# Performance work log

Measured on AMD Instinct MI355X. Metric: run time of the kernel, lower is better.

The kernel has to match this reference:

```python
import jax, jax.numpy as jnp
import numpy as np

B, S, N, H = 1024, 256, 64, 256
DA, DR = 350, 30  # attention dims W_s1 out, W_s2 out


def setup_inputs() -> dict:
    key = jax.random.key(0)
    ks = jax.random.split(key, 30)
    f32 = jnp.float32
    inp = {}
    inp['values'] = jax.random.normal(ks[0], (B, S, N), dtype=f32)
    inp['masks'] = (jax.random.uniform(ks[1], (B, S, N)) < 0.8).astype(f32)
    inp['deltas'] = jax.random.uniform(ks[2], (B, S, N), dtype=f32) * 5.0
    inp['labels'] = (jax.random.uniform(ks[3], (B,)) < 0.5).astype(f32)
    inp['is_train'] = (jax.random.uniform(ks[4], (B,)) < 0.9).astype(f32)

    def lin(k, o, i, s=0.05):
        kw, kb = jax.random.split(k)
        return (jax.random.normal(kw, (o, i), dtype=f32) * s,
                jax.random.normal(kb, (o,), dtype=f32) * s)

    inp['td_h_W'], inp['td_h_b'] = lin(ks[5], H, N)
    inp['td_x_W'], inp['td_x_b'] = lin(ks[6], N, N)
    inp['hist_W'], inp['hist_b'] = lin(ks[7], N, H)
    inp['feat_W'], inp['feat_b'] = lin(ks[8], N, N)
    inp['comb_W'], inp['comb_b'] = lin(ks[9], N, 2 * N)
    inp['W_ih'], inp['b_ih'] = lin(ks[10], 4 * H, 2 * N)
    inp['W_hh'], inp['b_hh'] = lin(ks[11], 4 * H, H)
    inp['Ws1_W'], inp['Ws1_b'] = lin(ks[12], DA, H)
    inp['Ws2_W'], inp['Ws2_b'] = lin(ks[13], DR, DA)
    inp['out_W'], inp['out_b'] = lin(ks[14], 1, DR * H)
    return inp


def reference(values, masks, deltas, labels, is_train,
              td_h_W, td_h_b, td_x_W, td_x_b,
              hist_W, hist_b, feat_W, feat_b,
              comb_W, comb_b, W_ih, W_hh, b_ih, b_hh,
              Ws1_W, Ws1_b, Ws2_W, Ws2_b, out_W, out_b):
    eye = jnp.eye(N, dtype=values.dtype)
    td_x_Wd = td_x_W * eye          # diag=True temporal decay
    feat_Wm = feat_W * (1.0 - eye)

    def step(carry, xs):
        h, c, xl = carry
        x, m, d = xs  # each [B, N]
        gamma_h = jnp.exp(-jax.nn.relu(d @ td_h_W.T + td_h_b))
        gamma_x = jnp.exp(-jax.nn.relu(d @ td_x_Wd.T + td_x_b))
        h = h * gamma_h
        x_h = h @ hist_W.T + hist_b
        msum = jnp.sum(m) + 1e-5
        xl = xl + jnp.sum(jnp.abs(x - x_h) * m) / msum
        x_c = m * x + (1.0 - m) * x_h
        z_h = x_c @ feat_Wm.T + feat_b
        xl = xl + jnp.sum(jnp.abs(x - z_h) * m) / msum
        alpha = jnp.concatenate([gamma_x, m], axis=1) @ comb_W.T + comb_b
        c_h = alpha * z_h + (1.0 - alpha) * x_h
        xl = xl + jnp.sum(jnp.abs(x - c_h) * m) / msum
        c_c = m * x + (1.0 - m) * c_h
        inp = jnp.concatenate([c_c, m], axis=1)
        gates = inp @ W_ih.T + b_ih + h @ W_hh.T + b_hh
        i_g, f_g, g_g, o_g = jnp.split(gates, 4, axis=1)  # torch LSTM gate order
        c = jax.nn.sigmoid(f_g) * c + jax.nn.sigmoid(i_g) * jnp.tanh(g_g)
        h = jax.nn.sigmoid(o_g) * jnp.tanh(c)
        return (h, c, xl), (h, c_c)

    h0 = jnp.zeros((B, H), dtype=values.dtype)
    c0 = jnp.zeros((B, H), dtype=values.dtype)
    xs = (values.transpose(1, 0, 2), masks.transpose(1, 0, 2), deltas.transpose(1, 0, 2))
    (_, _, x_loss), (Hs, imps) = jax.lax.scan(step, (h0, c0, jnp.zeros((), values.dtype)), xs)
    H_rnn = Hs.transpose(1, 0, 2)        # [B, S, H]
    imputations = imps.transpose(1, 0, 2)  # [B, S, N]

    # late attention
    scores = jnp.tanh(H_rnn @ Ws1_W.T + Ws1_b) @ Ws2_W.T + Ws2_b  # [B, S, DR]
    attn = jax.nn.softmax(scores.transpose(0, 2, 1), axis=2)       # [B, DR, S]
    hidden = jnp.einsum('brs,bsh->brh', attn, H_rnn)               # [B, DR, H]
    y_h = hidden.reshape(B, DR * H) @ out_W.T + out_b               # [B, 1]

    lab = labels.reshape(-1, 1)
    tr = is_train.reshape(-1, 1)
    bce = jax.nn.relu(y_h) - y_h * lab + jnp.log1p(jnp.exp(-jnp.abs(y_h)))
    y_loss = jnp.sum(bce * tr) / (jnp.sum(tr) + 1e-5)
    loss = x_loss / S + y_loss * 0.1
    predictions = jax.nn.sigmoid(y_h)
    return loss, predictions, imputations
```

## Files before the change

kernel.cpp:

```cpp
#include <hip/hip_runtime.h>
#include <hip/hip_bf16.h>
#include <math.h>


#define BB 1024
#define SS 256
#define NF 64
#define HD 256
#define DAA 350
#define DRR 30
#define RPB 4

#define WS_B5_OFS 4096
#define WS_B5_ELEMS (64 * 12 * 64 * 8)
#define WS_B6_OFS (WS_B5_OFS + WS_B5_ELEMS * 2)
#define WS_B6_ELEMS (22 * 8 * 64 * 8)
#define WS_B3_OFS (WS_B6_OFS + WS_B6_ELEMS * 2)
#define WS_B3_ELEMS (4 * 8 * 64 * 8)
#define WS_B2_OFS (WS_B3_OFS + WS_B3_ELEMS * 2)
#define WS_B2_ELEMS (16 * 2 * 64 * 8)
#define WS_B7_OFS (WS_B2_OFS + WS_B2_ELEMS * 2)
#define WS_B7_ELEMS (2 * 11 * 64 * 8)
#define CW_TOTAL (WS_B5_ELEMS + WS_B6_ELEMS + WS_B3_ELEMS + WS_B2_ELEMS + WS_B7_ELEMS)
#define WS_H_OFS (2 * 1024 * 1024)
#define WS_H_BYTES ((size_t)BB * SS * HD * 2)

typedef __attribute__((ext_vector_type(8))) short bf16x8;
typedef __attribute__((ext_vector_type(4))) float f32x4;

__device__ __forceinline__ float dot4f(float4 a, float4 b) {
  return fmaf(a.x, b.x, fmaf(a.y, b.y, fmaf(a.z, b.z, a.w * b.w)));
}

__device__ __forceinline__ short f2bs(float v) {
  __hip_bfloat16 t = __float2bfloat16(v);
  return *reinterpret_cast<short*>(&t);
}

__global__ __launch_bounds__(256) void convert_weights(
    const float* __restrict__ W_ih, const float* __restrict__ W_hh,
    const float* __restrict__ Ws1_W, const float* __restrict__ hist_W,
    const float* __restrict__ td_h_W, const float* __restrict__ Ws2_W,
    short* __restrict__ b5, short* __restrict__ b6,
    short* __restrict__ b3, short* __restrict__ b2, short* __restrict__ b7)
{
  int idx = blockIdx.x * 256 + threadIdx.x;
  if (idx < WS_B5_ELEMS) {
    int j = idx & 7; int e8 = idx >> 3; int lane = e8 & 63; int tile = e8 >> 6;
    int kt = tile % 12, nt = tile / 12;
    int g = nt * 16 + (lane & 15);
    int k = kt * 32 + (lane >> 4) * 8 + j;
    float v = (k < 128) ? W_ih[g * 128 + k] : W_hh[g * 256 + (k - 128)];
    b5[idx] = f2bs(v);
  } else if (idx < WS_B5_ELEMS + WS_B6_ELEMS) {
    int i = idx - WS_B5_ELEMS;
    int j = i & 7; int e8 = i >> 3; int lane = e8 & 63; int tile = e8 >> 6;
    int kt = tile & 7, nt = tile >> 3;
    int a = nt * 16 + (lane & 15);
    int k = kt * 32 + (lane >> 4) * 8 + j;
    float v = (a < DAA) ? Ws1_W[a * 256 + k] : 0.f;
    b6[i] = f2bs(v);
  } else if (idx < WS_B5_ELEMS + WS_B6_ELEMS + WS_B3_ELEMS) {
    int i = idx - WS_B5_ELEMS - WS_B6_ELEMS;
    int j = i & 7; int e8 = i >> 3; int lane = e8 & 63; int tile = e8 >> 6;
    int kt = tile & 7, nt = tile >> 3;
    int n = nt * 16 + (lane & 15);
    int k = kt * 32 + (lane >> 4) * 8 + j;
    b3[i] = f2bs(hist_W[n * 256 + k]);
  } else if (idx < WS_B5_ELEMS + WS_B6_ELEMS + WS_B3_ELEMS + WS_B2_ELEMS) {
    int i = idx - WS_B5_ELEMS - WS_B6_ELEMS - WS_B3_ELEMS;
    int j = i & 7; int e8 = i >> 3; int lane = e8 & 63; int tile = e8 >> 6;
    int kt = tile & 1, nt = tile >> 1;
    int g = nt * 16 + (lane & 15);
    int k = kt * 32 + (lane >> 4) * 8 + j;
    b2[i] = f2bs(td_h_W[g * 64 + k]);
  } else if (idx < CW_TOTAL) {
    int i = idx - WS_B5_ELEMS - WS_B6_ELEMS - WS_B3_ELEMS - WS_B2_ELEMS;
    int j = i & 7; int e8 = i >> 3; int lane = e8 & 63; int tile = e8 >> 6;
    int kt = tile % 11, nt = tile / 11;
    int r = nt * 16 + (lane & 15);
    int k = kt * 32 + (lane >> 4) * 8 + j;
    float v = (r < DRR && k < DAA) ? Ws2_W[r * DAA + k] : 0.f;
    b7[i] = f2bs(v);
  }
}

__global__ __launch_bounds__(256) void prep_kernel(
    const float* __restrict__ masks, const float* __restrict__ is_train,
    float* __restrict__ ws)
{
  __shared__ float red[256];
  const int t = blockIdx.x;
  const int tid = threadIdx.x;
  float s = 0.f;
  for (int idx = tid; idx < BB * NF; idx += 256) {
    int b = idx >> 6, n = idx & 63;
    s += masks[(size_t)b * (SS * NF) + (size_t)t * NF + n];
  }
  red[tid] = s;
  __syncthreads();
  for (int off = 128; off > 0; off >>= 1) {
    if (tid < off) red[tid] += red[tid + off];
    __syncthreads();
  }
  if (tid == 0) ws[16 + t] = red[0] + 1e-5f;
  if (blockIdx.x == 0) {
    __syncthreads();
    float ts = 0.f;
    for (int idx = tid; idx < BB; idx += 256) ts += is_train[idx];
    red[tid] = ts;
    __syncthreads();
    for (int off = 128; off > 0; off >>= 1) {
      if (tid < off) red[tid] += red[tid + off];
      __syncthreads();
    }
    if (tid == 0) { ws[2] = red[0]; ws[0] = 0.f; ws[1] = 0.f; }
  }
}

__global__ __launch_bounds__(512, 2) void rits_scan(
    const float* __restrict__ values, const float* __restrict__ masks_g,
    const float* __restrict__ deltas,
    const float* __restrict__ td_h_b, const float* __restrict__ td_x_W,
    const float* __restrict__ td_x_b, const float* __restrict__ hist_b,
    const float* __restrict__ feat_W, const float* __restrict__ feat_b,
    const float* __restrict__ comb_W, const float* __restrict__ comb_b,
    const float* __restrict__ b_ih, const float* __restrict__ b_hh,
    float* __restrict__ out, float* __restrict__ ws)
{
  __shared__ __align__(16) float sh_a[RPB][384];
  __shared__ __align__(16) short sh_ab[16][392];
  __shared__ __align__(16) short sh_db[16][72];
  __shared__ __align__(16) float sh_x[RPB][NF];
  __shared__ __align__(16) float sh_d[RPB][NF];
  __shared__ __align__(16) float sh_xc[RPB][NF];
  __shared__ __align__(16) float sh_gx[RPB][NF];
  __shared__ __align__(16) float sh_xh[RPB][NF];
  __shared__ __align__(16) float sh_gates[RPB][1024];
  __shared__ float sh_msum;

  const int tid = threadIdx.x;
  const int b0 = blockIdx.x * RPB;
  const int wv = tid >> 6;
  const int lane = tid & 63;
  const int lm = lane & 15;
  const int lq = lane >> 4;
  const int row = tid >> 7;
  const int j = tid & 127;
  const int jA = j, jB = j + 128;
  const int row2 = tid >> 6;
  const int nn = tid & 63;

  const bf16x8* b5 = (const bf16x8*)((const char*)ws + WS_B5_OFS);
  const bf16x8* b3 = (const bf16x8*)((const char*)ws + WS_B3_OFS);
  const bf16x8* b2 = (const bf16x8*)((const char*)ws + WS_B2_OFS);
  short* Hw = (short*)((char*)ws + WS_H_OFS);

  for (int i = tid; i < 16 * 392; i += 512) (&sh_ab[0][0])[i] = 0;
  for (int i = tid; i < 16 * 72; i += 512) (&sh_db[0][0])[i] = 0;
  for (int i = tid; i < RPB * 384; i += 512) (&sh_a[0][0])[i] = 0.f;

  const float tdxw  = td_x_W[nn * NF + nn];
  const float tdxb  = td_x_b[nn];
  const float featb = feat_b[nn];
  const float featd = feat_W[nn * NF + nn];
  const float combb = comb_b[nn];
  float bgA[4], bgB[4];
  #pragma unroll
  for (int q = 0; q < 4; ++q) {
    bgA[q] = b_ih[q * 256 + jA] + b_hh[q * 256 + jA];
    bgB[q] = b_ih[q * 256 + jB] + b_hh[q * 256 + jB];
  }
  float thb[2];
  thb[0] = td_h_b[(wv * 2 + 0) * 16 + lm];
  thb[1] = td_h_b[(wv * 2 + 1) * 16 + lm];
  float hbv = 0.f;
  if (wv < 4) hbv = hist_b[wv * 16 + lm];

  float cA = 0.f, cB = 0.f;
  double lossAcc = 0.0;

  float pv_a = 0.f, pv_b = 0.f, pv_msum = 0.f;
  if (tid < 256) {
    size_t g = (size_t)(b0 + row2) * (SS * NF) + nn;
    pv_a = values[g];
    pv_b = deltas[g];
  } else {
    int q = tid - 256; int rw = q >> 6, n2 = q & 63;
    size_t g = (size_t)(b0 + rw) * (SS * NF) + n2;
    pv_a = masks_g[g];
  }
  if (tid == 0) pv_msum = ws[16];

  __syncthreads();

  for (int t = 0; t < SS; ++t) {
    if (tid < 256) {
      sh_x[row2][nn] = pv_a;
      sh_d[row2][nn] = pv_b;
      sh_db[row2][nn] = f2bs(pv_b);
    } else {
      int q = tid - 256;
      int rw = q >> 6, n2 = q & 63;
      sh_a[rw][64 + n2] = pv_a;
      sh_ab[rw][64 + n2] = f2bs(pv_a);
    }
    if (tid == 0) sh_msum = pv_msum;
    __syncthreads();

    if (t + 1 < SS) {
      if (tid < 256) {
        size_t g = (size_t)(b0 + row2) * (SS * NF) + (size_t)(t + 1) * NF + nn;
        pv_a = values[g];
        pv_b = deltas[g];
      } else {
        int q = tid - 256; int rw = q >> 6, n2 = q & 63;
        size_t g = (size_t)(b0 + rw) * (SS * NF) + (size_t)(t + 1) * NF + n2;
        pv_a = masks_g[g];
      }
      if (tid == 0) pv_msum = ws[16 + t + 1];
    }

    {
      bf16x8 dfr[2];
      #pragma unroll
      for (int kt = 0; kt < 2; ++kt)
        dfr[kt] = *(const bf16x8*)(&sh_db[lm][0] + kt * 32 + lq * 8);
      #pragma unroll
      for (int ntl = 0; ntl < 2; ++ntl) {
        int nt = wv * 2 + ntl;
        f32x4 acc = {0.f, 0.f, 0.f, 0.f};
        const bf16x8* bp = b2 + (size_t)(nt * 2) * 64 + lane;
        acc = __builtin_amdgcn_mfma_f32_16x16x32_bf16(dfr[0], bp[0], acc, 0, 0, 0);
        acc = __builtin_amdgcn_mfma_f32_16x16x32_bf16(dfr[1], bp[64], acc, 0, 0, 0);
        if (lq == 0) {
          int g = nt * 16 + lm;
          float bias = thb[ntl];
          #pragma unroll
          for (int r = 0; r < 4; ++r) {
            float gam = expf(-fmaxf(acc[r] + bias, 0.f));
            float h = sh_a[r][128 + g] * gam;
            sh_a[r][128 + g] = h;
            sh_ab[r][128 + g] = f2bs(h);
          }
        }
      }
      if (tid < 256) {
        float v = sh_d[row2][nn] * tdxw + tdxb;
        sh_gx[row2][nn] = expf(-fmaxf(v, 0.f));
      }
    }
    __syncthreads();

    if (wv < 4) {
      int nt = wv;
      f32x4 acc = {0.f, 0.f, 0.f, 0.f};
      const bf16x8* bp = b3 + (size_t)(nt * 8) * 64 + lane;
      #pragma unroll
      for (int kt = 0; kt < 8; ++kt) {
        bf16x8 a = *(const bf16x8*)(&sh_ab[lm][128] + kt * 32 + lq * 8);
        acc = __builtin_amdgcn_mfma_f32_16x16x32_bf16(a, bp[kt * 64], acc, 0, 0, 0);
      }
      if (lq == 0) {
        int n = nt * 16 + lm;
        float lterm = 0.f;
        #pragma unroll
        for (int r = 0; r < 4; ++r) {
          float xh = acc[r] + hbv;
          sh_xh[r][n] = xh;
          float m = sh_a[r][64 + n], x = sh_x[r][n];
          sh_xc[r][n] = m * x + (1.f - m) * xh;
          lterm += fabsf(x - xh) * m;
        }
        lossAcc += (double)(lterm / sh_msum);
      }
    }
    __syncthreads();

    if (tid < 256) {
      const float4* xc4 = (const float4*)&sh_xc[row2][0];
      const float4* gx4 = (const float4*)&sh_gx[row2][0];
      const float4* mm4 = (const float4*)&sh_a[row2][64];
      const float4* fW  = (const float4*)(feat_W + nn * NF);
      const float4* cW0 = (const float4*)(comb_W + nn * 2 * NF);
      const float4* cW1 = (const float4*)(comb_W + nn * 2 * NF + NF);
      float az = 0.f, aa = 0.f;
      #pragma unroll
      for (int k = 0; k < 16; ++k) {
        az += dot4f(xc4[k], fW[k]);
        aa += dot4f(gx4[k], cW0[k]);
        aa += dot4f(mm4[k], cW1[k]);
      }
      float xcn = sh_xc[row2][nn];
      float zh = az - xcn * featd + featb;
      float alpha = aa + combb;
      float xh = sh_xh[row2][nn];
      float chv = alpha * zh + (1.f - alpha) * xh;
      float m = sh_a[row2][64 + nn], x = sh_x[row2][nn];
      float ccv = m * x + (1.f - m) * chv;
      sh_ab[row2][nn] = f2bs(ccv);
      out[1 + BB + ((size_t)(b0 + row2) * SS + t) * NF + nn] = ccv;
      float lsum = (fabsf(x - zh) + fabsf(x - chv)) * m;
      lossAcc += (double)(lsum / sh_msum);
    }
    __syncthreads();

    {
      bf16x8 afr[12];
      #pragma unroll
      for (int kt = 0; kt < 12; ++kt)
        afr[kt] = *(const bf16x8*)(&sh_ab[lm][0] + kt * 32 + lq * 8);
      #pragma unroll 2
      for (int ntl = 0; ntl < 8; ++ntl) {
        int nt = wv * 8 + ntl;
        f32x4 acc = {0.f, 0.f, 0.f, 0.f};
        const bf16x8* bp = b5 + (size_t)(nt * 12) * 64 + lane;
        #pragma unroll
        for (int kt = 0; kt < 12; ++kt)
          acc = __builtin_amdgcn_mfma_f32_16x16x32_bf16(afr[kt], bp[kt * 64], acc, 0, 0, 0);
        if (lq == 0) {
          int n = nt * 16 + lm;
          #pragma unroll
          for (int r = 0; r < 4; ++r) sh_gates[r][n] = acc[r];
        }
      }
    }
    __syncthreads();

    {
      float giA = sh_gates[row][jA] + bgA[0];
      float gfA = sh_gates[row][256 + jA] + bgA[1];
      float ggA = sh_gates[row][512 + jA] + bgA[2];
      float goA = sh_gates[row][768 + jA] + bgA[3];
      float iA = 1.f / (1.f + expf(-giA));
      float fA = 1.f / (1.f + expf(-gfA));
      float oA = 1.f / (1.f + expf(-goA));
      cA = fA * cA + iA * tanhf(ggA);
      float hnA = oA * tanhf(cA);
      float giB = sh_gates[row][jB] + bgB[0];
      float gfB = sh_gates[row][256 + jB] + bgB[1];
      float ggB = sh_gates[row][512 + jB] + bgB[2];
      float goB = sh_gates[row][768 + jB] + bgB[3];
      float iB = 1.f / (1.f + expf(-giB));
      float fB = 1.f / (1.f + expf(-gfB));
      float oB = 1.f / (1.f + expf(-goB));
      cB = fB * cB + iB * tanhf(ggB);
      float hnB = oB * tanhf(cB);
      short hA = f2bs(hnA), hB = f2bs(hnB);
      sh_a[row][128 + jA] = hnA;
      sh_a[row][128 + jB] = hnB;
      sh_ab[row][128 + jA] = hA;
      sh_ab[row][128 + jB] = hB;
      size_t hb = ((size_t)(b0 + row) * SS + t) * HD;
      Hw[hb + jA] = hA;
      Hw[hb + jB] = hB;
    }
  }

  float* sred = &sh_gates[0][0];
  __syncthreads();
  sred[tid] = (float)lossAcc;
  __syncthreads();
  for (int off = 256; off > 0; off >>= 1) {
    if (tid < off) sred[tid] += sred[tid + off];
    __syncthreads();
  }
  if (tid == 0) atomicAdd(&ws[0], sred[0]);
}

__global__ __launch_bounds__(256) void rits_attn(
    const float* __restrict__ labels, const float* __restrict__ is_train,
    const float* __restrict__ Ws1_b,
    const float* __restrict__ out_W, const float* __restrict__ out_b,
    float* __restrict__ out, float* __restrict__ ws)
{
  __shared__ __align__(16) short sh_s1[16][360];
  __shared__ __align__(16) float sh_sc[32][256];
  __shared__ __align__(16) short sh_at[32][264];

  const int tid = threadIdx.x;
  const int b = blockIdx.x;
  const int wv = tid >> 6;
  const int lane = tid & 63;
  const int lm = lane & 15;
  const int lq = lane >> 4;

  const bf16x8* b6 = (const bf16x8*)((const char*)ws + WS_B6_OFS);
  const bf16x8* b7 = (const bf16x8*)((const char*)ws + WS_B7_OFS);
  const ushort* Hg = (const ushort*)((const char*)ws + WS_H_OFS) + (size_t)b * SS * HD;

  for (int i = tid; i < 16 * 360; i += 256) (&sh_s1[0][0])[i] = 0;
  for (int i = tid; i < 32 * 264; i += 256) (&sh_at[0][0])[i] = 0;

  float w1b[6];
  #pragma unroll
  for (int i = 0; i < 6; ++i) {
    int nt = wv + 4 * i;
    int a = nt * 16 + lm;
    w1b[i] = (nt < 22 && a < DAA) ? Ws1_b[a] : 0.f;
  }
  __syncthreads();

  for (int sc0 = 0; sc0 < SS; sc0 += 16) {
    bf16x8 afr[8];
    const ushort* Hrow = Hg + (size_t)(sc0 + lm) * HD;
    #pragma unroll
    for (int kt = 0; kt < 8; ++kt)
      afr[kt] = *(const bf16x8*)(Hrow + kt * 32 + lq * 8);
    int i = 0;
    for (int nt = wv; nt < 22; nt += 4, ++i) {
      f32x4 acc = {0.f, 0.f, 0.f, 0.f};
      const bf16x8* bp = b6 + (size_t)(nt * 8) * 64 + lane;
      #pragma unroll
      for (int kt = 0; kt < 8; ++kt)
        acc = __builtin_amdgcn_mfma_f32_16x16x32_bf16(afr[kt], bp[kt * 64], acc, 0, 0, 0);
      int a = nt * 16 + lm;
      if (a < DAA) {
        float bias = w1b[i];
        #pragma unroll
        for (int r = 0; r < 4; ++r)
          sh_s1[lq * 4 + r][a] = f2bs(tanhf(acc[r] + bias));
      }
    }
    __syncthreads();
    if (wv < 2) {
      bf16x8 s1f[11];
      #pragma unroll
      for (int kt = 0; kt < 11; ++kt)
        s1f[kt] = *(const bf16x8*)(&sh_s1[lm][0] + kt * 32 + lq * 8);
      f32x4 acc = {0.f, 0.f, 0.f, 0.f};
      const bf16x8* bp = b7 + (size_t)(wv * 11) * 64 + lane;
      #pragma unroll
      for (int kt = 0; kt < 11; ++kt)
        acc = __builtin_amdgcn_mfma_f32_16x16x32_bf16(s1f[kt], bp[kt * 64], acc, 0, 0, 0);
      int r = wv * 16 + lm;
      if (r < DRR) {
        float4 v = {acc[0], acc[1], acc[2], acc[3]};
        *(float4*)&sh_sc[r][sc0 + lq * 4] = v;
      }
    }
    __syncthreads();
  }

  if (tid < 240) {
    int r = tid >> 3, g = tid & 7;
    float M = -1e30f;
    for (int s = g; s < SS; s += 8) M = fmaxf(M, sh_sc[r][s]);
    #pragma unroll
    for (int off = 1; off < 8; off <<= 1) M = fmaxf(M, __shfl_xor(M, off));
    float L = 0.f;
    for (int s = g; s < SS; s += 8) {
      float e = expf(sh_sc[r][s] - M);
      sh_sc[r][s] = e;
      L += e;
    }
    #pragma unroll
    for (int off = 1; off < 8; off <<= 1) L += __shfl_xor(L, off);
    float inv = 1.f / L;
    for (int s = g; s < SS; s += 8) sh_at[r][s] = f2bs(sh_sc[r][s] * inv);
  }
  __syncthreads();

  bf16x8 aat[2][8];
  #pragma unroll
  for (int mt = 0; mt < 2; ++mt)
    #pragma unroll
    for (int kt = 0; kt < 8; ++kt)
      aat[mt][kt] = *(const bf16x8*)(&sh_at[mt * 16 + lm][0] + kt * 32 + lq * 8);

  float p = 0.f;
  #pragma unroll
  for (int ntl = 0; ntl < 4; ++ntl) {
    int nt = wv * 4 + ntl;
    f32x4 acc0 = {0.f, 0.f, 0.f, 0.f};
    f32x4 acc1 = {0.f, 0.f, 0.f, 0.f};
    #pragma unroll
    for (int kt = 0; kt < 8; ++kt) {
      const ushort* hp = Hg + (size_t)(kt * 32 + lq * 8) * HD + nt * 16 + lm;
      bf16x8 bf;
      #pragma unroll
      for (int jj = 0; jj < 8; ++jj) bf[jj] = (short)hp[(size_t)jj * HD];
      acc0 = __builtin_amdgcn_mfma_f32_16x16x32_bf16(aat[0][kt], bf, acc0, 0, 0, 0);
      acc1 = __builtin_amdgcn_mfma_f32_16x16x32_bf16(aat[1][kt], bf, acc1, 0, 0, 0);
    }
    int h = nt * 16 + lm;
    #pragma unroll
    for (int ri = 0; ri < 4; ++ri) {
      int r0 = lq * 4 + ri;
      p += out_W[r0 * HD + h] * acc0[ri];
      int r1 = 16 + lq * 4 + ri;
      if (r1 < DRR) p += out_W[r1 * HD + h] * acc1[ri];
    }
  }

  float* sred = &sh_sc[0][0];
  __syncthreads();
  sred[tid] = p;
  __syncthreads();
  for (int off = 128; off > 0; off >>= 1) {
    if (tid < off) sred[tid] += sred[tid + off];
    __syncthreads();
  }
  if (tid == 0) {
    float yh = sred[0] + out_b[0];
    float lab = labels[b], tr = is_train[b];
    float bce = fmaxf(yh, 0.f) - yh * lab + log1pf(expf(-fabsf(yh)));
    atomicAdd(&ws[1], bce * tr);
    out[1 + b] = 1.f / (1.f + expf(-yh));
  }
}

__global__ __launch_bounds__(512, 2) void rits_fused(
    const float* __restrict__ values, const float* __restrict__ masks_g,
    const float* __restrict__ deltas, const float* __restrict__ labels,
    const float* __restrict__ is_train,
    const float* __restrict__ td_h_b, const float* __restrict__ td_x_W,
    const float* __restrict__ td_x_b, const float* __restrict__ hist_b,
    const float* __restrict__ feat_W, const float* __restrict__ feat_b,
    const float* __restrict__ comb_W, const float* __restrict__ comb_b,
    const float* __restrict__ b_ih, const float* __restrict__ b_hh,
    const float* __restrict__ Ws1_b,
    const float* __restrict__ Ws2_W, const float* __restrict__ Ws2_b,
    const float* __restrict__ out_W, const float* __restrict__ out_b,
    float* __restrict__ out, float* __restrict__ ws)
{
  __shared__ __align__(16) float sh_a[4][384];
  __shared__ __align__(16) short sh_ab[16][392];
  __shared__ __align__(16) short sh_db[16][72];
  __shared__ __align__(16) float sh_x[4][NF];
  __shared__ __align__(16) float sh_d[4][NF];
  __shared__ __align__(16) float sh_xc[4][NF];
  __shared__ __align__(16) float sh_gx[4][NF];
  __shared__ __align__(16) float sh_xh[4][NF];
  __shared__ __align__(16) float sh_gates[4][1024];
  __shared__ __align__(16) float sh_s1[4][352];
  __shared__ float sh_w[4][32];
  __shared__ float sh_scale[4][32];
  __shared__ float sh_M[4][32];
  __shared__ float sh_L[4][32];
  __shared__ float sh_msum;

  const int tid = threadIdx.x;
  const int b0 = blockIdx.x * 4;
  const int wv = tid >> 6;
  const int lane = tid & 63;
  const int lm = lane & 15;
  const int lq = lane >> 4;
  const int row = tid >> 7;
  const int j = tid & 127;
  const int jA = j, jB = j + 128;
  const int row2 = tid >> 6;
  const int nn = tid & 63;

  const bf16x8* b5 = (const bf16x8*)((const char*)ws + WS_B5_OFS);
  const bf16x8* b6 = (const bf16x8*)((const char*)ws + WS_B6_OFS);
  const bf16x8* b3 = (const bf16x8*)((const char*)ws + WS_B3_OFS);
  const bf16x8* b2 = (const bf16x8*)((const char*)ws + WS_B2_OFS);

  for (int i = tid; i < 16 * 392; i += 512) (&sh_ab[0][0])[i] = 0;
  for (int i = tid; i < 16 * 72; i += 512) (&sh_db[0][0])[i] = 0;
  for (int i = tid; i < 4 * 384; i += 512) (&sh_a[0][0])[i] = 0.f;
  if (tid < 128) {
    int rr = tid >> 5, q = tid & 31;
    sh_M[rr][q] = -1e30f;
    sh_L[rr][q] = 0.f;
  }

  const float tdxw  = td_x_W[nn * NF + nn];
  const float tdxb  = td_x_b[nn];
  const float featb = feat_b[nn];
  const float featd = feat_W[nn * NF + nn];
  const float combb = comb_b[nn];
  float bgA[4], bgB[4];
  #pragma unroll
  for (int q = 0; q < 4; ++q) {
    bgA[q] = b_ih[q * 256 + jA] + b_hh[q * 256 + jA];
    bgB[q] = b_ih[q * 256 + jB] + b_hh[q * 256 + jB];
  }

  float cA = 0.f, cB = 0.f;
  float OA[DRR], OBv[DRR];
  #pragma unroll
  for (int r = 0; r < DRR; ++r) { OA[r] = 0.f; OBv[r] = 0.f; }
  double lossAcc = 0.0;

  __syncthreads();

  for (int t = 0; t < SS; ++t) {
    if (tid < 256) {
      size_t g = (size_t)(b0 + row2) * (SS * NF) + (size_t)t * NF + nn;
      float xv = values[g], dv = deltas[g];
      sh_x[row2][nn] = xv;
      sh_d[row2][nn] = dv;
      sh_db[row2][nn] = f2bs(dv);
    } else {
      int q = tid - 256;
      int rw = q >> 6, n2 = q & 63;
      size_t g = (size_t)(b0 + rw) * (SS * NF) + (size_t)t * NF + n2;
      float mv = masks_g[g];
      sh_a[rw][64 + n2] = mv;
      sh_ab[rw][64 + n2] = f2bs(mv);
    }
    if (tid == 0) sh_msum = ws[16 + t];
    __syncthreads();

    {
      bf16x8 dfr[2];
      #pragma unroll
      for (int kt = 0; kt < 2; ++kt)
        dfr[kt] = *(const bf16x8*)(&sh_db[lm][0] + kt * 32 + lq * 8);
      #pragma unroll
      for (int ntl = 0; ntl < 2; ++ntl) {
        int nt = wv * 2 + ntl;
        f32x4 acc = {0.f, 0.f, 0.f, 0.f};
        const bf16x8* bp = b2 + (size_t)(nt * 2) * 64 + lane;
        acc = __builtin_amdgcn_mfma_f32_16x16x32_bf16(dfr[0], bp[0], acc, 0, 0, 0);
        acc = __builtin_amdgcn_mfma_f32_16x16x32_bf16(dfr[1], bp[64], acc, 0, 0, 0);
        if (lq == 0) {
          int g = nt * 16 + lm;
          float bias = td_h_b[g];
          #pragma unroll
          for (int r = 0; r < 4; ++r) {
            float gam = expf(-fmaxf(acc[r] + bias, 0.f));
            float h = sh_a[r][128 + g] * gam;
            sh_a[r][128 + g] = h;
            sh_ab[r][128 + g] = f2bs(h);
          }
        }
      }
      if (tid < 256) {
        float v = sh_d[row2][nn] * tdxw + tdxb;
        sh_gx[row2][nn] = expf(-fmaxf(v, 0.f));
      }
    }
    __syncthreads();

    if (wv < 4) {
      int nt = wv;
      f32x4 acc = {0.f, 0.f, 0.f, 0.f};
      const bf16x8* bp = b3 + (size_t)(nt * 8) * 64 + lane;
      #pragma unroll
      for (int kt = 0; kt < 8; ++kt) {
        bf16x8 a = *(const bf16x8*)(&sh_ab[lm][128] + kt * 32 + lq * 8);
        acc = __builtin_amdgcn_mfma_f32_16x16x32_bf16(a, bp[kt * 64], acc, 0, 0, 0);
      }
      if (lq == 0) {
        int n = nt * 16 + lm;
        float bias = hist_b[n];
        float lterm = 0.f;
        #pragma unroll
        for (int r = 0; r < 4; ++r) {
          float xh = acc[r] + bias;
          sh_xh[r][n] = xh;
          float m = sh_a[r][64 + n], x = sh_x[r][n];
          sh_xc[r][n] = m * x + (1.f - m) * xh;
          lterm += fabsf(x - xh) * m;
        }
        lossAcc += (double)(lterm / sh_msum);
      }
    }
    __syncthreads();

    if (tid < 256) {
      const float4* xc4 = (const float4*)&sh_xc[row2][0];
      const float4* gx4 = (const float4*)&sh_gx[row2][0];
      const float4* mm4 = (const float4*)&sh_a[row2][64];
      const float4* fW  = (const float4*)(feat_W + nn * NF);
      const float4* cW0 = (const float4*)(comb_W + nn * 2 * NF);
      const float4* cW1 = (const float4*)(comb_W + nn * 2 * NF + NF);
      float az = 0.f, aa = 0.f;
      #pragma unroll
      for (int k = 0; k < 16; ++k) {
        az += dot4f(xc4[k], fW[k]);
        aa += dot4f(gx4[k], cW0[k]);
        aa += dot4f(mm4[k], cW1[k]);
      }
      float xcn = sh_xc[row2][nn];
      float zh = az - xcn * featd + featb;
      float alpha = aa + combb;
      float xh = sh_xh[row2][nn];
      float chv = alpha * zh + (1.f - alpha) * xh;
      float m = sh_a[row2][64 + nn], x = sh_x[row2][nn];
      float ccv = m * x + (1.f - m) * chv;
      sh_ab[row2][nn] = f2bs(ccv);
      out[1 + BB + ((size_t)(b0 + row2) * SS + t) * NF + nn] = ccv;
      float lsum = (fabsf(x - zh) + fabsf(x - chv)) * m;
      lossAcc += (double)(lsum / sh_msum);
    }
    __syncthreads();

    {
      bf16x8 afr[12];
      #pragma unroll
      for (int kt = 0; kt < 12; ++kt)
        afr[kt] = *(const bf16x8*)(&sh_ab[lm][0] + kt * 32 + lq * 8);
      #pragma unroll 2
      for (int ntl = 0; ntl < 8; ++ntl) {
        int nt = wv * 8 + ntl;
        f32x4 acc = {0.f, 0.f, 0.f, 0.f};
        const bf16x8* bp = b5 + (size_t)(nt * 12) * 64 + lane;
        #pragma unroll
        for (int kt = 0; kt < 12; ++kt)
          acc = __builtin_amdgcn_mfma_f32_16x16x32_bf16(afr[kt], bp[kt * 64], acc, 0, 0, 0);
        if (lq == 0) {
          int n = nt * 16 + lm;
          #pragma unroll
          for (int r = 0; r < 4; ++r) sh_gates[r][n] = acc[r];
        }
      }
    }
    __syncthreads();

    float hnA, hnB;
    {
      float giA = sh_gates[row][jA] + bgA[0];
      float gfA = sh_gates[row][256 + jA] + bgA[1];
      float ggA = sh_gates[row][512 + jA] + bgA[2];
      float goA = sh_gates[row][768 + jA] + bgA[3];
      float iA = 1.f / (1.f + expf(-giA));
      float fA = 1.f / (1.f + expf(-gfA));
      float oA = 1.f / (1.f + expf(-goA));
      cA = fA * cA + iA * tanhf(ggA);
      hnA = oA * tanhf(cA);
      float giB = sh_gates[row][jB] + bgB[0];
      float gfB = sh_gates[row][256 + jB] + bgB[1];
      float ggB = sh_gates[row][512 + jB] + bgB[2];
      float goB = sh_gates[row][768 + jB] + bgB[3];
      float iB = 1.f / (1.f + expf(-giB));
      float fB = 1.f / (1.f + expf(-gfB));
      float oB = 1.f / (1.f + expf(-goB));
      cB = fB * cB + iB * tanhf(ggB);
      hnB = oB * tanhf(cB);
      sh_a[row][128 + jA] = hnA;
      sh_a[row][128 + jB] = hnB;
      sh_ab[row][128 + jA] = f2bs(hnA);
      sh_ab[row][128 + jB] = f2bs(hnB);
    }
    __syncthreads();

    {
      bf16x8 hfr[8];
      #pragma unroll
      for (int kt = 0; kt < 8; ++kt)
        hfr[kt] = *(const bf16x8*)(&sh_ab[lm][128] + kt * 32 + lq * 8);
      for (int nt = wv; nt < 22; nt += 8) {
        f32x4 acc = {0.f, 0.f, 0.f, 0.f};
        const bf16x8* bp = b6 + (size_t)(nt * 8) * 64 + lane;
        #pragma unroll
        for (int kt = 0; kt < 8; ++kt)
          acc = __builtin_amdgcn_mfma_f32_16x16x32_bf16(hfr[kt], bp[kt * 64], acc, 0, 0, 0);
        if (lq == 0) {
          int a = nt * 16 + lm;
          if (a < DAA) {
            float bias = Ws1_b[a];
            #pragma unroll
            for (int r = 0; r < 4; ++r) sh_s1[r][a] = tanhf(acc[r] + bias);
          }
        }
      }
    }
    __syncthreads();

    if (tid < 4 * DRR) {
      int rw = tid / DRR;
      int r = tid - rw * DRR;
      const float2* s2 = (const float2*)&sh_s1[rw][0];
      const float2* w2 = (const float2*)(Ws2_W + (size_t)r * DAA);
      float acc = 0.f;
      #pragma unroll 5
      for (int k = 0; k < 175; ++k) {
        float2 a = s2[k], b = w2[k];
        acc = fmaf(a.x, b.x, fmaf(a.y, b.y, acc));
      }
      float sc = acc + Ws2_b[r];
      float Mo = sh_M[rw][r];
      float Mn = fmaxf(Mo, sc);
      float scl = expf(Mo - Mn);
      float w = expf(sc - Mn);
      sh_M[rw][r] = Mn;
      sh_L[rw][r] = sh_L[rw][r] * scl + w;
      sh_scale[rw][r] = scl;
      sh_w[rw][r] = w;
    }
    __syncthreads();

    #pragma unroll
    for (int r = 0; r < DRR; ++r) {
      float scl = sh_scale[row][r];
      float w = sh_w[row][r];
      OA[r]  = OA[r]  * scl + w * hnA;
      OBv[r] = OBv[r] * scl + w * hnB;
    }
  }

  float pA = 0.f, pB = 0.f;
  #pragma unroll
  for (int r = 0; r < DRR; ++r) {
    float invL = 1.f / sh_L[row][r];
    pA += out_W[r * HD + jA] * (OA[r]  * invL);
    pB += out_W[r * HD + jB] * (OBv[r] * invL);
  }
  float* sred = &sh_s1[0][0];
  __syncthreads();
  sred[row * 256 + jA] = pA;
  sred[row * 256 + jB] = pB;
  __syncthreads();
  if (tid < 4) {
    float acc = 0.f;
    for (int k = 0; k < 256; ++k) acc += sred[tid * 256 + k];
    float yh = acc + out_b[0];
    int b = b0 + tid;
    float lab = labels[b], tr = is_train[b];
    float bce = fmaxf(yh, 0.f) - yh * lab + log1pf(expf(-fabsf(yh)));
    atomicAdd(&ws[1], bce * tr);
    out[1 + b] = 1.f / (1.f + expf(-yh));
  }
  __syncthreads();
  sred[tid] = (float)lossAcc;
  __syncthreads();
  for (int off = 256; off > 0; off >>= 1) {
    if (tid < off) sred[tid] += sred[tid + off];
    __syncthreads();
  }
  if (tid == 0) atomicAdd(&ws[0], sred[0]);
}

__global__ void final_kernel(const float* __restrict__ ws, float* __restrict__ out) {
  if (threadIdx.x == 0 && blockIdx.x == 0) {
    out[0] = ws[0] / (float)SS + 0.1f * (ws[1] / (ws[2] + 1e-5f));
  }
}

extern "C" void kernel_launch(void* const* d_in, const int* in_sizes, int n_in,
                              void* d_out, int out_size, void* d_ws, size_t ws_size,
                              hipStream_t stream) {
  const float* values   = (const float*)d_in[0];
  const float* masks    = (const float*)d_in[1];
  const float* deltas   = (const float*)d_in[2];
  const float* labels   = (const float*)d_in[3];
  const float* is_train = (const float*)d_in[4];
  const float* td_h_W   = (const float*)d_in[5];
  const float* td_h_b   = (const float*)d_in[6];
  const float* td_x_W   = (const float*)d_in[7];
  const float* td_x_b   = (const float*)d_in[8];
  const float* hist_W   = (const float*)d_in[9];
  const float* hist_b   = (const float*)d_in[10];
  const float* feat_W   = (const float*)d_in[11];
  const float* feat_b   = (const float*)d_in[12];
  const float* comb_W   = (const float*)d_in[13];
  const float* comb_b   = (const float*)d_in[14];
  const float* W_ih     = (const float*)d_in[15];
  const float* b_ih     = (const float*)d_in[16];
  const float* W_hh     = (const float*)d_in[17];
  const float* b_hh     = (const float*)d_in[18];
  const float* Ws1_W    = (const float*)d_in[19];
  const float* Ws1_b    = (const float*)d_in[20];
  const float* Ws2_W    = (const float*)d_in[21];
  const float* Ws2_b    = (const float*)d_in[22];
  const float* out_W    = (const float*)d_in[23];
  const float* out_b    = (const float*)d_in[24];
  float* out = (float*)d_out;
  float* ws  = (float*)d_ws;

  short* b5 = (short*)((char*)d_ws + WS_B5_OFS);
  short* b6 = (short*)((char*)d_ws + WS_B6_OFS);
  short* b3 = (short*)((char*)d_ws + WS_B3_OFS);
  short* b2 = (short*)((char*)d_ws + WS_B2_OFS);
  short* b7 = (short*)((char*)d_ws + WS_B7_OFS);

  convert_weights<<<(CW_TOTAL + 255) / 256, 256, 0, stream>>>(
      W_ih, W_hh, Ws1_W, hist_W, td_h_W, Ws2_W, b5, b6, b3, b2, b7);
  prep_kernel<<<SS, 256, 0, stream>>>(masks, is_train, ws);

  if (ws_size >= (size_t)WS_H_OFS + WS_H_BYTES) {
    rits_scan<<<BB / RPB, 512, 0, stream>>>(
        values, masks, deltas,
        td_h_b, td_x_W, td_x_b, hist_b, feat_W, feat_b, comb_W, comb_b,
        b_ih, b_hh, out, ws);
    rits_attn<<<BB, 256, 0, stream>>>(
        labels, is_train, Ws1_b, out_W, out_b, out, ws);
  } else {
    rits_fused<<<BB / 4, 512, 0, stream>>>(
        values, masks, deltas, labels, is_train,
        td_h_b, td_x_W, td_x_b, hist_b, feat_W, feat_b, comb_W, comb_b,
        b_ih, b_hh, Ws1_b, Ws2_W, Ws2_b, out_W, out_b, out, ws);
  }
  final_kernel<<<1, 64, 0, stream>>>(ws, out);
}
```

Measured before the change: 4.545 ms.

## Compute next-step hidden decay one step ahead and drop per-step barriers

Deltas are now prefetched two steps ahead so the temporal-decay gamma for step t+1 is computed during step t. The decay is applied to the new hidden state right in the LSTM epilogue, and the next step's x, mask and decay inputs are staged in shared memory at the end of each step. This removes the separate staging barrier and the barrier after the decay stage, which shortens the per-timestep critical path of the sequential scan. The fp32 hidden-state copy in shared memory is dropped, but there is an extra shared gamma buffer, more live registers and a subtler cross-step ordering that must be kept correct.

```diff
diff --git a/kernel.cpp b/kernel.cpp
--- a/kernel.cpp
+++ b/kernel.cpp
@@ -128,14 +128,14 @@
     const float* __restrict__ b_ih, const float* __restrict__ b_hh,
     float* __restrict__ out, float* __restrict__ ws)
 {
-  __shared__ __align__(16) float sh_a[RPB][384];
   __shared__ __align__(16) short sh_ab[16][392];
   __shared__ __align__(16) short sh_db[16][72];
   __shared__ __align__(16) float sh_x[RPB][NF];
-  __shared__ __align__(16) float sh_d[RPB][NF];
+  __shared__ __align__(16) float sh_m[RPB][NF];
   __shared__ __align__(16) float sh_xc[RPB][NF];
   __shared__ __align__(16) float sh_gx[RPB][NF];
   __shared__ __align__(16) float sh_xh[RPB][NF];
+  __shared__ __align__(16) float sh_gam[RPB][HD];
   __shared__ __align__(16) float sh_gates[RPB][1024];
   __shared__ float sh_msum;
 
@@ -158,7 +158,6 @@
 
   for (int i = tid; i < 16 * 392; i += 512) (&sh_ab[0][0])[i] = 0;
   for (int i = tid; i < 16 * 72; i += 512) (&sh_db[0][0])[i] = 0;
-  for (int i = tid; i < RPB * 384; i += 512) (&sh_a[0][0])[i] = 0.f;
 
   const float tdxw  = td_x_W[nn * NF + nn];
   const float tdxb  = td_x_b[nn];
@@ -180,43 +179,36 @@
   float cA = 0.f, cB = 0.f;
   double lossAcc = 0.0;
 
-  float pv_a = 0.f, pv_b = 0.f, pv_msum = 0.f;
+  float pv_x = 0.f, pv_m = 0.f, pv_d2 = 0.f, pv_msum = 0.f;
   if (tid < 256) {
     size_t g = (size_t)(b0 + row2) * (SS * NF) + nn;
-    pv_a = values[g];
-    pv_b = deltas[g];
+    sh_x[row2][nn] = values[g];
+    float d0 = deltas[g];
+    sh_gx[row2][nn] = expf(-fmaxf(d0 * tdxw + tdxb, 0.f));
+    float d1 = deltas[g + NF];
+    sh_db[row2][nn] = f2bs(d1);
+    pv_d2 = d1;
   } else {
     int q = tid - 256; int rw = q >> 6, n2 = q & 63;
     size_t g = (size_t)(b0 + rw) * (SS * NF) + n2;
-    pv_a = masks_g[g];
-  }
-  if (tid == 0) pv_msum = ws[16];
-
+    float mv = masks_g[g];
+    sh_m[rw][n2] = mv;
+    sh_ab[rw][64 + n2] = f2bs(mv);
+  }
+  if (tid == 0) sh_msum = ws[16];
   __syncthreads();
 
   for (int t = 0; t < SS; ++t) {
-    if (tid < 256) {
-      sh_x[row2][nn] = pv_a;
-      sh_d[row2][nn] = pv_b;
-      sh_db[row2][nn] = f2bs(pv_b);
-    } else {
-      int q = tid - 256;
-      int rw = q >> 6, n2 = q & 63;
-      sh_a[rw][64 + n2] = pv_a;
-      sh_ab[rw][64 + n2] = f2bs(pv_a);
-    }
-    if (tid == 0) sh_msum = pv_msum;
-    __syncthreads();
-
+    float pv_d1 = pv_d2;
     if (t + 1 < SS) {
       if (tid < 256) {
         size_t g = (size_t)(b0 + row2) * (SS * NF) + (size_t)(t + 1) * NF + nn;
-        pv_a = values[g];
-        pv_b = deltas[g];
+        pv_x = values[g];
+        if (t + 2 < SS) pv_d2 = deltas[g + NF];
       } else {
         int q = tid - 256; int rw = q >> 6, n2 = q & 63;
         size_t g = (size_t)(b0 + rw) * (SS * NF) + (size_t)(t + 1) * NF + n2;
-        pv_a = masks_g[g];
+        pv_m = masks_g[g];
       }
       if (tid == 0) pv_msum = ws[16 + t + 1];
     }
@@ -237,20 +229,11 @@
           int g = nt * 16 + lm;
           float bias = thb[ntl];
           #pragma unroll
-          for (int r = 0; r < 4; ++r) {
-            float gam = expf(-fmaxf(acc[r] + bias, 0.f));
-            float h = sh_a[r][128 + g] * gam;
-            sh_a[r][128 + g] = h;
-            sh_ab[r][128 + g] = f2bs(h);
-          }
+          for (int r = 0; r < 4; ++r)
+            sh_gam[r][g] = expf(-fmaxf(acc[r] + bias, 0.f));
         }
       }
-      if (tid < 256) {
-        float v = sh_d[row2][nn] * tdxw + tdxb;
-        sh_gx[row2][nn] = expf(-fmaxf(v, 0.f));
-      }
-    }
-    __syncthreads();
+    }
 
     if (wv < 4) {
       int nt = wv;
@@ -268,7 +251,7 @@
         for (int r = 0; r < 4; ++r) {
           float xh = acc[r] + hbv;
           sh_xh[r][n] = xh;
-          float m = sh_a[r][64 + n], x = sh_x[r][n];
+          float m = sh_m[r][n], x = sh_x[r][n];
           sh_xc[r][n] = m * x + (1.f - m) * xh;
           lterm += fabsf(x - xh) * m;
         }
@@ -280,7 +263,7 @@
     if (tid < 256) {
       const float4* xc4 = (const float4*)&sh_xc[row2][0];
       const float4* gx4 = (const float4*)&sh_gx[row2][0];
-      const float4* mm4 = (const float4*)&sh_a[row2][64];
+      const float4* mm4 = (const float4*)&sh_m[row2][0];
       const float4* fW  = (const float4*)(feat_W + nn * NF);
       const float4* cW0 = (const float4*)(comb_W + nn * 2 * NF);
       const float4* cW1 = (const float4*)(comb_W + nn * 2 * NF + NF);
@@ -296,7 +279,7 @@
       float alpha = aa + combb;
       float xh = sh_xh[row2][nn];
       float chv = alpha * zh + (1.f - alpha) * xh;
-      float m = sh_a[row2][64 + nn], x = sh_x[row2][nn];
+      float m = sh_m[row2][nn], x = sh_x[row2][nn];
       float ccv = m * x + (1.f - m) * chv;
       sh_ab[row2][nn] = f2bs(ccv);
       out[1 + BB + ((size_t)(b0 + row2) * SS + t) * NF + nn] = ccv;
@@ -346,19 +329,30 @@
       float oB = 1.f / (1.f + expf(-goB));
       cB = fB * cB + iB * tanhf(ggB);
       float hnB = oB * tanhf(cB);
-      short hA = f2bs(hnA), hB = f2bs(hnB);
-      sh_a[row][128 + jA] = hnA;
-      sh_a[row][128 + jB] = hnB;
-      sh_ab[row][128 + jA] = hA;
-      sh_ab[row][128 + jB] = hB;
       size_t hb = ((size_t)(b0 + row) * SS + t) * HD;
-      Hw[hb + jA] = hA;
-      Hw[hb + jB] = hB;
-    }
+      Hw[hb + jA] = f2bs(hnA);
+      Hw[hb + jB] = f2bs(hnB);
+      float hdA = hnA * sh_gam[row][jA];
+      float hdB = hnB * sh_gam[row][jB];
+      sh_ab[row][128 + jA] = f2bs(hdA);
+      sh_ab[row][128 + jB] = f2bs(hdB);
+    }
+    if (t + 1 < SS) {
+      if (tid < 256) {
+        sh_x[row2][nn] = pv_x;
+        sh_gx[row2][nn] = expf(-fmaxf(pv_d1 * tdxw + tdxb, 0.f));
+        sh_db[row2][nn] = f2bs(pv_d2);
+      } else {
+        int q = tid - 256; int rw = q >> 6, n2 = q & 63;
+        sh_m[rw][n2] = pv_m;
+        sh_ab[rw][64 + n2] = f2bs(pv_m);
+      }
+      if (tid == 0) sh_msum = pv_msum;
+    }
+    __syncthreads();
   }
 
   float* sred = &sh_gates[0][0];
-  __syncthreads();
   sred[tid] = (float)lossAcc;
   __syncthreads();
   for (int off = 256; off > 0; off >>= 1) {
```

Measured after the change: 4.364 ms. 4.0% less time.
